# Performance work log

Hardware: AMD Instinct MI355X
Metric: run time of the kernel (lower is better)

## Reference

```python
import jax, jax.numpy as jnp
import numpy as np

# dims matching init_kwargs
L, D, NH = 4, 1024, 16          # num_blocks, embed_dim, num_heads
HD = D // NH                     # head dim
CUR, MEM, BS, IN = 512, 512, 8, 512
FF = 4 * D
GRU_BIAS = 2.0

def sinusoidal_pe(full_seq, dim):
    # SinusoidalPE: freqs = arange(0, dim, 2); inv = 10000**(-freqs/dim); seq descending
    freqs = jnp.arange(0, dim, 2.0)
    inv = 10000.0 ** (-freqs / dim)
    seq = jnp.arange(full_seq - 1, -1, -1.0)
    ang = seq[:, None] * inv[None, :]                       # (full, dim/2)
    return jnp.concatenate([jnp.sin(ang), jnp.cos(ang)], axis=-1)  # (full, dim)

def layer_norm(x, g, b, eps=1e-5):
    m = x.mean(-1, keepdims=True)
    v = ((x - m) ** 2).mean(-1, keepdims=True)
    return (x - m) * jax.lax.rsqrt(v + eps) * g + b

def rel_shift(x):
    # Transformer-XL relative shift. x: (q, k, b, h)
    q, k, b, h = x.shape
    zp = jnp.zeros((q, 1, b, h), x.dtype)
    return jnp.concatenate([zp, x], axis=1).reshape(k + 1, q, b, h)[1:].reshape(q, k, b, h)

def gru_gate(x, y, W):
    # W: (6, D, D) = Wr, Ur, Wz, Uz, Wg, Ug (no bias except learned-ish gru_bias on z)
    Wr, Ur, Wz, Uz, Wg, Ug = W[0], W[1], W[2], W[3], W[4], W[5]
    r = jax.nn.sigmoid(y @ Wr.T + x @ Ur.T)
    z = jax.nn.sigmoid(y @ Wz.T + x @ Uz.T - GRU_BIAS)
    hh = jnp.tanh(y @ Wg.T + (r * x) @ Ug.T)
    return (1.0 - z) * x + z * hh

def rel_attn(q, k, v, pos, U, V, mask, W):
    # q: (cur, bs, D); k, v: (full, bs, D); pos: (full, D); W: (5, D, D) = Wq,Wk,Wv,Wr,Wo
    cur, bs, _ = q.shape
    full = k.shape[0]
    qh = (q @ W[0].T).reshape(cur, bs, NH, HD)
    kh = (k @ W[1].T).reshape(full, bs, NH, HD)
    vh = (v @ W[2].T).reshape(full, bs, NH, HD)
    rh = (pos @ W[3].T).reshape(full, NH, HD)
    AC = jnp.einsum('ibhd,jbhd->ijbh', qh + U, kh)          # content stream with U bias
    BD = rel_shift(jnp.einsum('ibhd,jhd->ijbh', qh + V, rh))  # position stream with V bias
    score = (AC + BD) * (1.0 / np.sqrt(HD))
    score = jnp.where(mask[:, :, None, None], jnp.asarray(-1e30, score.dtype), score)
    attn = jax.nn.softmax(score, axis=1)
    out = jnp.einsum('ijbh,jbhd->ibhd', attn, vh).reshape(cur, bs, D)
    return out @ W[4].T

def gelu(x):
    return jax.nn.gelu(x, approximate=False)  # torch nn.GELU default is exact

def _forward(h, memory, W_emb, b_emb, U, V, ln1, ln2, Wattn, g1, g2, fc_W1, fc_b1, fc_W2, fc_b2):
    h = jnp.transpose(h, (1, 0, 2))            # (cur, bs, in)
    mem = jax.lax.stop_gradient(memory)        # memory holds detached hidden states
    cur = h.shape[0]
    prev = mem.shape[1]
    full = cur + prev
    x = gelu(h @ W_emb.T + b_emb)              # linear embedding + GELU activation
    pos = sinusoidal_pe(full, D)               # (full, D); pos_emb.unsqueeze(1) broadcast over bs
    mask = jnp.triu(jnp.ones((cur, full), bool), 1 + prev)
    out = x
    for i in range(L):
        key = jnp.concatenate([mem[i], out], axis=0)   # (full, bs, D)
        nq = layer_norm(out, ln1[i, 0], ln1[i, 1])
        nk = layer_norm(key, ln1[i, 0], ln1[i, 1])
        Y = rel_attn(nq, nk, nk, pos, U, V, mask, Wattn[i])
        Y = gelu(Y)                                     # dropout is identity (eval / p=0)
        o1 = gru_gate(out, Y, g1[i])
        E = layer_norm(o1, ln2[i, 0], ln2[i, 1])
        E = gelu(gelu(E @ fc_W1[i].T + fc_b1[i]) @ fc_W2[i].T + fc_b2[i])
        out = gru_gate(o1, E, g2[i])
    return jnp.transpose(out, (1, 0, 2))       # (bs, cur, D)

def setup_inputs() -> dict:
    key = jax.random.key(0)
    ks = jax.random.split(key, 12)
    s = 0.02
    eye2 = jnp.stack([jnp.ones(D, jnp.float32), jnp.zeros(D, jnp.float32)])  # (gamma, beta)
    return {
        'h': jax.random.normal(ks[0], (BS, CUR, IN), jnp.float32),
        'memory': jax.random.normal(ks[1], (L, MEM, BS, D), jnp.float32),
        'W_emb': jax.random.normal(ks[2], (D, IN), jnp.float32) * s,
        'b_emb': jnp.zeros((D,), jnp.float32),
        'U': jax.random.normal(ks[3], (NH, HD), jnp.float32) * s,
        'V': jax.random.normal(ks[4], (NH, HD), jnp.float32) * s,
        'ln1': jnp.tile(eye2[None], (L, 1, 1)),
        'ln2': jnp.tile(eye2[None], (L, 1, 1)),
        'Wattn': jax.random.normal(ks[5], (L, 5, D, D), jnp.float32) * s,  # q,k,v,r,o per block
        'g1': jax.random.normal(ks[6], (L, 6, D, D), jnp.float32) * s,
        'g2': jax.random.normal(ks[7], (L, 6, D, D), jnp.float32) * s,
        'fc_W1': jax.random.normal(ks[8], (L, FF, D), jnp.float32) * s,
        'fc_b1': jnp.zeros((L, FF), jnp.float32),
        'fc_W2': jax.random.normal(ks[9], (L, D, FF), jnp.float32) * s,
        'fc_b2': jnp.zeros((L, D), jnp.float32),
    }

def reference(h, memory, W_emb, b_emb, U, V, ln1, ln2, Wattn, g1, g2, fc_W1, fc_b1, fc_W2, fc_b2):
    return _forward(h, memory, W_emb, b_emb, U, V, ln1, ln2, Wattn, g1, g2, fc_W1, fc_b1, fc_W2, fc_b2)
```

## Files before the change

### kernel.cpp

```cpp
#include <hip/hip_runtime.h>
#include <hip/hip_bf16.h>


typedef __attribute__((ext_vector_type(8))) __bf16 bfrag;
typedef __attribute__((ext_vector_type(4))) float f4;
typedef __attribute__((ext_vector_type(4))) unsigned short u16x4;
typedef __attribute__((ext_vector_type(8))) unsigned short u16x8;

__device__ __forceinline__ unsigned short f2bf(float f){
  union { float f; unsigned u; } v; v.f = f;
  unsigned r = v.u + 0x7fffu + ((v.u >> 16) & 1u);
  return (unsigned short)(r >> 16);
}
__device__ __forceinline__ float bf2f(unsigned short u){
  union { unsigned u; float f; } v; v.u = (unsigned)u << 16; return v.f;
}
__device__ __forceinline__ float geluf(float x){
  return 0.5f * x * (1.0f + erff(x * 0.7071067811865476f));
}
__device__ __forceinline__ float sigm(float x){ return 1.0f/(1.0f + __expf(-x)); }

__device__ __forceinline__ void gl_lds(const void* g, void* l){
  __builtin_amdgcn_global_load_lds(
    reinterpret_cast<const __attribute__((address_space(1))) unsigned int*>(
        reinterpret_cast<unsigned long>(g)),
    reinterpret_cast<__attribute__((address_space(3))) unsigned int*>(
        reinterpret_cast<unsigned long>(l)),
    16, 0, 0);
}

struct GP {
  const unsigned short* A;
  const unsigned short* A2;
  const unsigned short* B;
  const unsigned short* B2;
  unsigned short* O1;
  unsigned short* O2;
  unsigned short* O3;
  unsigned short* O4;
  unsigned short* O5;
  float* OF;
  const float* bias1;
  const float* bias2;
  const float* X;
  const float* Z;
  int K, Ksplit, lda, ldb, ldo;
  int sBz;
};

template<int BM, int BN, int EPI>
__global__ __launch_bounds__(256) void gemm_k(GP p){
  __shared__ unsigned short As[2][2][BM*32];
  __shared__ unsigned short Bs[2][2][BN*32];
  const int tid  = threadIdx.x;
  const int lane = tid & 63;
  const int wid  = tid >> 6;
  const int lr   = lane & 15;
  const int lg   = lane >> 4;
  constexpr int FM = BM/32, FN = BN/32;

  int bx = blockIdx.x, by = blockIdx.y;
  {
    const int gx = gridDim.x;
    const int nwg = gx * gridDim.y;
    if ((nwg & 7) == 0){
      const int bid = by*gx + bx;
      const int vid = (bid & 7)*(nwg >> 3) + (bid >> 3);
      bx = vid % gx;
      by = vid / gx;
    }
  }
  const int m0 = by * BM;
  const int n0 = bx * BN;
  const int z  = blockIdx.z;

  const unsigned short* Abase = p.A;
  const unsigned short* Bbase = p.B;
  if constexpr (EPI==13){
    if (z==2){ if (by >= 32) return; Abase = p.A + 4194304; }
    if (z==3){ if (by >= 8)  return; Abase = p.A2; }
    const int zsel = (z==0)?1:((z==1)?2:((z==2)?0:3));
    Bbase = p.B + (long)zsel*1048576;
  }

  const int ksp = p.Ksplit ? p.Ksplit : p.K;
  const unsigned short* AbL = Abase + (long)m0*p.lda;
  const unsigned short* AbH = p.A2 && EPI!=13 ? (p.A2 + (long)m0*p.lda - ksp) : AbL;
  const unsigned short* BbL = Bbase + (long)z*p.sBz + (long)n0*p.ldb;
  const unsigned short* BbH = p.B2 ? (p.B2 + (long)z*p.sBz + (long)n0*p.ldb - ksp) : BbL;

  const int srow = tid >> 2;
  const int skk  = (tid & 3) * 8;

  f4 acc[FM][FN];
  f4 zero4 = {0.0f, 0.0f, 0.0f, 0.0f};
  #pragma unroll
  for (int m=0;m<FM;m++)
    #pragma unroll
    for (int n=0;n<FN;n++) acc[m][n] = zero4;

  auto stage = [&](int buf, int sub, int k0){
    const unsigned short* A_ = (k0 < ksp) ? AbL : AbH;
    #pragma unroll
    for (int q=0;q<BM/64;q++)
      gl_lds(A_ + (long)(q*64 + srow)*p.lda + k0 + skk, (char*)As[buf][sub] + q*4096 + wid*1024);
    const unsigned short* B_ = (k0 < ksp) ? BbL : BbH;
    #pragma unroll
    for (int q=0;q<BN/64;q++)
      gl_lds(B_ + (long)(q*64 + srow)*p.ldb + k0 + skk, (char*)Bs[buf][sub] + q*4096 + wid*1024);
  };

  const int nk2 = p.K >> 6;
  stage(0,0,0); stage(0,1,32);
  __syncthreads();

  int cur = 0;
  for (int t = 0; t < nk2; ++t){
    if (t+1 < nk2){
      stage(cur^1, 0, (t+1)*64);
      stage(cur^1, 1, (t+1)*64 + 32);
    }
    #pragma unroll
    for (int sub=0; sub<2; ++sub){
      bfrag af[FM], bfr[FN];
      #pragma unroll
      for (int m=0;m<FM;m++)
        af[m] = *(const bfrag*)&As[cur][sub][((wid>>1)*(BM/2) + m*16 + lr)*32 + lg*8];
      #pragma unroll
      for (int n=0;n<FN;n++)
        bfr[n] = *(const bfrag*)&Bs[cur][sub][((wid&1)*(BN/2) + n*16 + lr)*32 + lg*8];
      #pragma unroll
      for (int m=0;m<FM;m++)
        #pragma unroll
        for (int n=0;n<FN;n++)
          acc[m][n] = __builtin_amdgcn_mfma_f32_16x16x32_bf16(af[m], bfr[n], acc[m][n], 0, 0, 0);
    }
    __syncthreads();
    cur ^= 1;
  }

  const int wr0 = m0 + (wid>>1)*(BM/2);
  const int wc0 = n0 + (wid&1)*(BN/2);
  #pragma unroll
  for (int m=0;m<FM;m++)
    #pragma unroll
    for (int n=0;n<FN;n++)
      #pragma unroll
      for (int r=0;r<4;r++){
        const int gr = wr0 + m*16 + lg*4 + r;
        const int gc = wc0 + n*16 + lr;
        const float a = acc[m][n][r];
        const long base = (long)gr*p.ldo + gc;
        if constexpr (EPI==6){
          const float t = a + (p.bias1 ? p.bias1[gc] : 0.0f);
          p.O1[base] = f2bf(geluf(t));
        }
        else if constexpr (EPI==7){
          const float t = geluf(a + p.bias1[gc]);
          p.OF[base] = t; p.O1[base] = f2bf(t);
        }
        else if constexpr (EPI==11){
          const long ix = (long)gr*1024 + gc;
          if (z==0) p.O1[ix] = f2bf(sigm(a) * p.X[ix]);
          else      p.OF[ix] = sigm(a - 2.0f);
        }
        else if constexpr (EPI==12){
          const long ix = (long)gr*1024 + gc;
          const float zz = p.Z[ix];
          const float oo = (1.0f - zz)*p.X[ix] + zz*tanhf(a);
          p.OF[ix] = oo; p.O1[ix] = f2bf(oo);
        }
        else if constexpr (EPI==13){
          const long ix = (long)gr*1024 + gc;
          if (z==0){ p.O1[ix] = f2bf(a); }
          else if (z==1){
            const int b_ = gr & 7, js = gr >> 3, h_ = gc >> 6, d_ = gc & 63;
            p.O2[(long)(b_*16 + h_)*65536 + (long)d_*1024 + js] = f2bf(a);
          }
          else if (z==2){ p.O3[ix] = f2bf((a + p.bias1[gc])*0.125f);
                          p.O4[ix] = f2bf((a + p.bias2[gc])*0.125f); }
          else { p.O5[ix] = f2bf(a); }
        }
      }
}

__global__ __launch_bounds__(256,3) void attn_k(const unsigned short* __restrict__ qU,
                                                const unsigned short* __restrict__ qV,
                                                const unsigned short* __restrict__ kh,
                                                const unsigned short* __restrict__ rh,
                                                const unsigned short* __restrict__ vhT,
                                                unsigned short* __restrict__ ctx){
  __shared__ char Sm[20480];
  __shared__ float redm[4][16];
  __shared__ float reds[4][16];
  __shared__ float invd[16];
  const int tid = threadIdx.x;
  const int w   = tid >> 6;
  const int lane= tid & 63;
  const int lr  = lane & 15;
  const int lg  = lane >> 4;
  const int id = blockIdx.x;
  const int b  = id & 7;
  const int i0 = ((id >> 3) & 31) * 16;
  const int h  = id >> 8;
  const int gmax = i0 >> 4;
  const long hoff = (long)h * 64;
  const f4 z4 = {0.f,0.f,0.f,0.f};

  bfrag bqv[2];
  #pragma unroll
  for (int kk=0;kk<2;kk++)
    bqv[kk] = *(const bfrag*)(qV + ((long)(i0 + lr)*8 + b)*1024 + hoff + kk*32 + lg*8);
  bfrag aq[2];
  #pragma unroll
  for (int kk=0;kk<2;kk++)
    aq[kk] = *(const bfrag*)(qU + ((long)(i0 + lr)*8 + b)*1024 + hoff + kk*32 + lg*8);

  const int nv1 = (gmax >= w) ? (((gmax - w) >> 2) + 1) : 0;

  f4 s[16];

#define LDK(DST, n_) { \
    const int cbx = c0 + (w + 4*(n_))*16; \
    DST[0] = *(const bfrag*)(kh + ((long)(cbx + lr)*8 + b)*1024 + hoff + lg*8); \
    DST[1] = *(const bfrag*)(kh + ((long)(cbx + lr)*8 + b)*1024 + hoff + 32 + lg*8); }

#define AC_CMP(n_, CUR) { \
    const int cbx = c0 + (w + 4*(n_))*16; \
    f4 a = z4; \
    __builtin_amdgcn_s_setprio(1); \
    a = __builtin_amdgcn_mfma_f32_16x16x32_bf16(aq[0], CUR[0], a, 0,0,0); \
    a = __builtin_amdgcn_mfma_f32_16x16x32_bf16(aq[1], CUR[1], a, 0,0,0); \
    __builtin_amdgcn_s_setprio(0); \
    _Pragma("unroll") \
    for (int q=0;q<4;q++){ \
      const int di = lg*4 + q; \
      const int jc = cbx + lr; \
      if (jc > i0 + di + 512) a[q] = -1e30f; \
      else { \
        const int rr = jc - di + radd; \
        a[q] += bf2f(*(const unsigned short*)(Sm + rr*38 + di*2)); \
      } \
    } \
    s[half*8 + n_] = a; }

#define AC_STEP(n_, CUR, NXT) \
    if ((n_)+2 < nv) LDK(NXT, (n_)+2); \
    if ((n_) < nv) AC_CMP(n_, CUR) \
    else s[half*8 + n_] = (f4){-1e30f,-1e30f,-1e30f,-1e30f};

  #pragma unroll
  for (int half=0; half<2; ++half){
    const int c0    = half*512;
    const int rbase = half ? (1008 - i0) : (496 - i0);
    const int ntil  = half ? (gmax + 1) : 33;
    const int radd  = half ? -497 : 15;
    for (int mt = w; mt < ntil; mt += 4){
      const int r0 = rbase + mt*16;
      f4 acc = z4;
      #pragma unroll
      for (int kk=0;kk<2;kk++){
        bfrag ar = *(const bfrag*)(rh + (long)(r0 + lr)*1024 + hoff + kk*32 + lg*8);
        acc = __builtin_amdgcn_mfma_f32_16x16x32_bf16(ar, bqv[kk], acc, 0,0,0);
      }
      #pragma unroll
      for (int q=0;q<4;q++){
        const int rr = mt*16 + lg*4 + q;
        *(unsigned short*)(Sm + rr*38 + lr*2) = f2bf(acc[q]);
      }
    }
    __syncthreads();
    const int nv = (half==0) ? 8 : nv1;
    {
      bfrag bkA[2], bkB[2], bkC[2];
      if (0 < nv) LDK(bkA, 0);
      if (1 < nv) LDK(bkB, 1);
      AC_STEP(0, bkA, bkC)
      AC_STEP(1, bkB, bkA)
      AC_STEP(2, bkC, bkB)
      AC_STEP(3, bkA, bkC)
      AC_STEP(4, bkB, bkA)
      AC_STEP(5, bkC, bkB)
      AC_STEP(6, bkA, bkC)
      AC_STEP(7, bkB, bkA)
    }
    __syncthreads();
  }

  const unsigned short* vb_base = vhT + (long)(b*16 + h)*65536;

#define LDV(DST, t_) { \
    const int c0v = ((t_) >> 2) * 512; \
    const int tau = (t_) & 3; \
    const int jA = c0v + (w + 8*tau)*16; \
    const int jB = c0v + (w + 8*tau + 4)*16; \
    const int jcol = (lg < 2) ? (jA + lg*8) : (jB + (lg-2)*8); \
    _Pragma("unroll") \
    for (int nd=0; nd<4; nd++) \
      DST[nd] = *(const bfrag*)(vb_base + (long)(nd*16 + lr)*1024 + jcol); }

#define CHV(t_) ((t_) < 4 || (2*((t_)-4) < nv1))

  bfrag vbA[4], vbB[4];
  LDV(vbA, 0);

  float mx[4], sum[4];
  #pragma unroll
  for (int q=0;q<4;q++){
    float m = s[0][q];
    #pragma unroll
    for (int n=1;n<16;n++) m = fmaxf(m, s[n][q]);
    m = fmaxf(m, __shfl_xor(m, 1));
    m = fmaxf(m, __shfl_xor(m, 2));
    m = fmaxf(m, __shfl_xor(m, 4));
    m = fmaxf(m, __shfl_xor(m, 8));
    if (lr == 0) redm[w][lg*4+q] = m;
  }
  __syncthreads();
  #pragma unroll
  for (int q=0;q<4;q++){
    const int row = lg*4+q;
    mx[q] = fmaxf(fmaxf(redm[0][row], redm[1][row]), fmaxf(redm[2][row], redm[3][row]));
    sum[q] = 0.0f;
  }
  #pragma unroll
  for (int n=0;n<16;n++)
    #pragma unroll
    for (int q=0;q<4;q++){
      const float e = __expf(s[n][q] - mx[q]);
      s[n][q] = e;
      sum[q] += e;
    }
  #pragma unroll
  for (int q=0;q<4;q++){
    float v = sum[q];
    v += __shfl_xor(v, 1);
    v += __shfl_xor(v, 2);
    v += __shfl_xor(v, 4);
    v += __shfl_xor(v, 8);
    if (lr == 0) reds[w][lg*4+q] = v;
  }
  __syncthreads();
  if (tid < 16)
    invd[tid] = 1.0f / (reds[0][tid] + reds[1][tid] + reds[2][tid] + reds[3][tid]);

  f4 oac[4];
  #pragma unroll
  for (int nd=0;nd<4;nd++) oac[nd] = z4;
  char* Pch = Sm + w*1024;

#define PV_STEP(t_, CUR, NXT) \
    if ((t_)+1 < 8 && CHV((t_)+1)) LDV(NXT, (t_)+1); \
    if (CHV(t_)){ \
      const int s0i = (((t_)<4)?0:8) + ((t_)&3)*2; \
      _Pragma("unroll") \
      for (int nn=0;nn<2;nn++){ \
        const f4 e = s[s0i + nn]; \
        _Pragma("unroll") \
        for (int q=0;q<4;q++){ \
          const int row = lg*4 + q; \
          const int col = nn*16 + lr; \
          *(unsigned short*)(Pch + row*64 + ((col*2) ^ (((row>>2)&3)<<4))) = f2bf(e[q]); \
        } \
      } \
      bfrag pa = *(const bfrag*)(Pch + lr*64 + ((lg*16) ^ (((lr>>2)&3)<<4))); \
      __builtin_amdgcn_s_setprio(1); \
      _Pragma("unroll") \
      for (int nd=0;nd<4;nd++) \
        oac[nd] = __builtin_amdgcn_mfma_f32_16x16x32_bf16(pa, CUR[nd], oac[nd], 0,0,0); \
      __builtin_amdgcn_s_setprio(0); \
    }

  PV_STEP(0, vbA, vbB)
  PV_STEP(1, vbB, vbA)
  PV_STEP(2, vbA, vbB)
  PV_STEP(3, vbB, vbA)
  PV_STEP(4, vbA, vbB)
  PV_STEP(5, vbB, vbA)
  PV_STEP(6, vbA, vbB)
  PV_STEP(7, vbB, vbA)

  float* po = (float*)(Sm + 4096 + w*4096);
  #pragma unroll
  for (int nd=0;nd<4;nd++)
    #pragma unroll
    for (int q=0;q<4;q++)
      po[(lg*4+q)*64 + nd*16 + lr] = oac[nd][q];
  __syncthreads();
  {
    const int row = tid >> 4;
    const int d0  = (tid & 15) * 4;
    f4 v = *(const f4*)(Sm + 4096 + (row*64 + d0)*4);
    #pragma unroll
    for (int ww=1;ww<4;ww++){
      const f4 u = *(const f4*)(Sm + 4096 + ww*4096 + (row*64 + d0)*4);
      v.x += u.x; v.y += u.y; v.z += u.z; v.w += u.w;
    }
    const float iv = invd[row];
    u16x4 o;
    o.x = f2bf(v.x*iv); o.y = f2bf(v.y*iv); o.z = f2bf(v.z*iv); o.w = f2bf(v.w*iv);
    *(u16x4*)(ctx + ((long)(i0 + row)*8 + b)*1024 + hoff + d0) = o;
  }
#undef LDK
#undef AC_CMP
#undef AC_STEP
#undef LDV
#undef CHV
#undef PV_STEP
}

__global__ __launch_bounds__(256) void ln_k(const float* __restrict__ srcA,
                                            const float* __restrict__ srcB, int splitRow,
                                            const float* __restrict__ g, const float* __restrict__ b,
                                            unsigned short* __restrict__ dst){
  const int row = blockIdx.x;
  const float* src = (srcB != nullptr && row >= splitRow)
                       ? (srcB + (long)(row - splitRow)*1024)
                       : (srcA + (long)row*1024);
  const int t = threadIdx.x;
  float4 v = ((const float4*)src)[t];
  float s1 = v.x+v.y+v.z+v.w;
  float s2 = v.x*v.x+v.y*v.y+v.z*v.z+v.w*v.w;
  #pragma unroll
  for (int o=32;o;o>>=1){ s1 += __shfl_xor(s1,o); s2 += __shfl_xor(s2,o); }
  __shared__ float r1[4], r2[4];
  const int w = t>>6;
  if ((t&63)==0){ r1[w]=s1; r2[w]=s2; }
  __syncthreads();
  s1 = r1[0]+r1[1]+r1[2]+r1[3];
  s2 = r2[0]+r2[1]+r2[2]+r2[3];
  const float mean = s1*(1.0f/1024.0f);
  const float var  = s2*(1.0f/1024.0f) - mean*mean;
  const float rs   = rsqrtf(var + 1e-5f);
  float4 gg = ((const float4*)g)[t];
  float4 bb = ((const float4*)b)[t];
  u16x4 o;
  o.x = f2bf((v.x-mean)*rs*gg.x + bb.x);
  o.y = f2bf((v.y-mean)*rs*gg.y + bb.y);
  o.z = f2bf((v.z-mean)*rs*gg.z + bb.z);
  o.w = f2bf((v.w-mean)*rs*gg.w + bb.w);
  *(u16x4*)(dst + (long)row*1024 + t*4) = o;
}

__global__ __launch_bounds__(256) void conv_k(const float* __restrict__ s,
                                              unsigned short* __restrict__ d, long n){
  long i = ((long)blockIdx.x*256 + threadIdx.x)*4;
  if (i >= n) return;
  float4 v = *(const float4*)(s + i);
  u16x4 o; o.x=f2bf(v.x); o.y=f2bf(v.y); o.z=f2bf(v.z); o.w=f2bf(v.w);
  *(u16x4*)(d + i) = o;
}

__global__ __launch_bounds__(256) void conv5_k(const float* __restrict__ wat,
                                               const float* __restrict__ g1,
                                               const float* __restrict__ g2,
                                               const float* __restrict__ f1,
                                               const float* __restrict__ f2,
                                               unsigned short* __restrict__ dst){
  const long i = ((long)blockIdx.x*256 + threadIdx.x)*4;
  const float* s; long off;
  if      (i <  5242880){ s = wat; off = 0; }
  else if (i < 11534336){ s = g1;  off = 5242880; }
  else if (i < 17825792){ s = g2;  off = 11534336; }
  else if (i < 22020096){ s = f1;  off = 17825792; }
  else                  { s = f2;  off = 22020096; }
  float4 v = *(const float4*)(s + (i - off));
  u16x4 o; o.x=f2bf(v.x); o.y=f2bf(v.y); o.z=f2bf(v.z); o.w=f2bf(v.w);
  *(u16x4*)(dst + i) = o;
}

__global__ __launch_bounds__(128) void ht_k(const float* __restrict__ h,
                                            unsigned short* __restrict__ d){
  const int row = blockIdx.x;
  const int i = row>>3, b = row&7;
  const float* src = h + ((long)b*512 + i)*512;
  const int t = threadIdx.x;
  float4 v = ((const float4*)src)[t];
  u16x4 o; o.x=f2bf(v.x); o.y=f2bf(v.y); o.z=f2bf(v.z); o.w=f2bf(v.w);
  *(u16x4*)(d + (long)row*512 + t*4) = o;
}

__global__ __launch_bounds__(256) void pos_k(unsigned short* __restrict__ d){
  const int r = blockIdx.x, t = threadIdx.x;
  const float seq = (float)(1023 - r);
  u16x4 o;
  #pragma unroll
  for (int q=0;q<4;q++){
    const int c = t*4 + q;
    const int f = (c < 512) ? c : (c - 512);
    const float inv = expf((float)f * -0.017988946039016f);
    const float ang = seq * inv;
    const float val = (c < 512) ? sinf(ang) : cosf(ang);
    o[q] = f2bf(val);
  }
  *(u16x4*)(d + (long)r*1024 + t*4) = o;
}

__global__ __launch_bounds__(256) void outT_k(const float* __restrict__ o,
                                              float* __restrict__ d){
  const int row = blockIdx.x;
  const int b = row>>9, i = row&511;
  const float4 v = ((const float4*)(o + ((long)i*8 + b)*1024))[threadIdx.x];
  ((float4*)(d + (long)row*1024))[threadIdx.x] = v;
}

extern "C" void kernel_launch(void* const* d_in, const int* in_sizes, int n_in,
                              void* d_out, int out_size, void* d_ws, size_t ws_size,
                              hipStream_t stream){
  (void)in_sizes; (void)n_in; (void)out_size; (void)ws_size;
  const float* h     = (const float*)d_in[0];
  const float* memin = (const float*)d_in[1];
  const float* Wemb  = (const float*)d_in[2];
  const float* bemb  = (const float*)d_in[3];
  const float* Ub    = (const float*)d_in[4];
  const float* Vb    = (const float*)d_in[5];
  const float* ln1   = (const float*)d_in[6];
  const float* ln2   = (const float*)d_in[7];
  const float* Wattn = (const float*)d_in[8];
  const float* g1w   = (const float*)d_in[9];
  const float* g2w   = (const float*)d_in[10];
  const float* fw1   = (const float*)d_in[11];
  const float* fb1   = (const float*)d_in[12];
  const float* fw2   = (const float*)d_in[13];
  const float* fb2   = (const float*)d_in[14];

  char* Wp = (char*)d_ws;
  size_t off = 0;
  auto take = [&](size_t bytes)->size_t{ size_t r = off; off += (bytes + 255) & ~(size_t)255; return r; };
  float*          outf = (float*)         (Wp + take(16777216));
  unsigned short* xbf  = (unsigned short*)(Wp + take( 8388608));
  float*          o1f  = (float*)         (Wp + take(16777216));
  unsigned short* o1b  = (unsigned short*)(Wp + take( 8388608));
  float*          zbf  = (float*)         (Wp + take(16777216));
  unsigned short* rxb  = (unsigned short*)(Wp + take( 8388608));
  unsigned short* yb   = (unsigned short*)(Wp + take( 8388608));
  unsigned short* Eb   = (unsigned short*)(Wp + take( 8388608));
  unsigned short* wb0  = (unsigned short*)(Wp + take(52428800));
  unsigned short* hTb  = (unsigned short*)(Wp + take( 4194304));
  unsigned short* webb = (unsigned short*)(Wp + take( 1048576));
  unsigned short* posb = (unsigned short*)(Wp + take( 2097152));
  unsigned short* nkb  = (unsigned short*)(Wp + take(16777216));
  unsigned short* qUb  = (unsigned short*)(Wp + take( 8388608));
  unsigned short* qVb  = (unsigned short*)(Wp + take( 8388608));
  unsigned short* khb  = (unsigned short*)(Wp + take(16777216));
  unsigned short* vhTb = (unsigned short*)(Wp + take(16777216));
  unsigned short* F1b  = khb;
  unsigned short* rhb  = (unsigned short*)(Wp + take( 2097152));
  unsigned short* ctxb = (unsigned short*)(Wp + take( 8388608));

  const int M1 = 1048576;

  conv_k<<<512, 256, 0, stream>>>(Wemb, webb, 524288);
  ht_k<<<4096, 128, 0, stream>>>(h, hTb);
  pos_k<<<1024, 256, 0, stream>>>(posb);

  {
    GP p{}; p.A=hTb; p.B=webb; p.OF=outf; p.O1=xbf; p.bias1=bemb;
    p.K=512; p.lda=512; p.ldb=512; p.ldo=1024;
    gemm_k<128,64,7><<<dim3(16,32,1),256,0,stream>>>(p);
  }

  auto gru_fn = [&](const unsigned short* xb, const float* xf, const unsigned short* yb_,
                    const unsigned short* w6, float* of, unsigned short* ob){
    { GP p{}; p.A=yb_; p.A2=xb; p.B=w6; p.B2=w6+M1; p.sBz=2*M1;
      p.O1=rxb; p.OF=zbf; p.X=xf;
      p.K=2048; p.Ksplit=1024; p.lda=1024; p.ldb=1024; p.ldo=1024;
      gemm_k<128,64,11><<<dim3(16,32,2),256,0,stream>>>(p); }
    { GP p{}; p.A=yb_; p.A2=rxb; p.B=w6+4*M1; p.B2=w6+5*M1;
      p.X=xf; p.Z=zbf; p.OF=of; p.O1=ob;
      p.K=2048; p.Ksplit=1024; p.lda=1024; p.ldb=1024; p.ldo=1024;
      gemm_k<128,64,12><<<dim3(16,32,1),256,0,stream>>>(p); }
  };

  for (int l = 0; l < 4; ++l){
    conv5_k<<<25600,256,0,stream>>>(Wattn + (long)l*5242880,
                                    g1w   + (long)l*6291456,
                                    g2w   + (long)l*6291456,
                                    fw1   + (long)l*4194304,
                                    fw2   + (long)l*4194304, wb0);

    ln_k<<<8192,256,0,stream>>>(memin + (long)l*4194304, outf, 4096,
                                ln1 + l*2048, ln1 + l*2048 + 1024, nkb);

    {
      GP p{}; p.A=nkb; p.A2=posb; p.B=wb0;
      p.O1=khb; p.O2=vhTb; p.O3=qUb; p.O4=qVb; p.O5=rhb;
      p.bias1=Ub; p.bias2=Vb;
      p.K=1024; p.lda=1024; p.ldb=1024; p.ldo=1024;
      gemm_k<128,64,13><<<dim3(16,64,4),256,0,stream>>>(p); }

    attn_k<<<4096,256,0,stream>>>(qUb, qVb, khb, rhb, vhTb, ctxb);

    {
      GP p{}; p.A=ctxb; p.B=wb0+4*M1; p.O1=yb;
      p.K=1024; p.lda=1024; p.ldb=1024; p.ldo=1024;
      gemm_k<128,64,6><<<dim3(16,32,1),256,0,stream>>>(p); }

    gru_fn(xbf, outf, yb, wb0 + 5*M1, o1f, o1b);

    ln_k<<<4096,256,0,stream>>>(o1f, nullptr, 1<<30,
                                ln2 + l*2048, ln2 + l*2048 + 1024, Eb);

    { GP p{}; p.A=Eb;  p.B=wb0+17*M1; p.O1=F1b; p.bias1=fb1 + l*4096;
      p.K=1024; p.lda=1024; p.ldb=1024; p.ldo=4096;
      gemm_k<128,64,6><<<dim3(64,32,1),256,0,stream>>>(p); }
    { GP p{}; p.A=F1b; p.B=wb0+21*M1; p.O1=yb; p.bias1=fb2 + l*1024;
      p.K=4096; p.lda=4096; p.ldb=4096; p.ldo=1024;
      gemm_k<128,64,6><<<dim3(16,32,1),256,0,stream>>>(p); }

    gru_fn(o1b, o1f, yb, wb0 + 11*M1, outf, xbf);
  }

  outT_k<<<4096,256,0,stream>>>(outf, (float*)d_out);
}
```

Measured before the change: 2.693 ms.

## Keep residual stream in bf16 and fuse final transpose into GRU epilogue

The fp32 copies of the residual stream (outf, o1f) and the z gate are replaced by bf16 buffers. GRU epilogues and layer norms now read bf16. The last GRU gate writes the transposed fp32 output straight to the result buffer, so the separate transpose kernel goes away. This cuts memory traffic in the epilogues and the LN loads, but the residual path now carries bf16 rounding across all layers, which can hurt accuracy.

```diff
diff --git a/kernel.cpp b/kernel.cpp
--- a/kernel.cpp
+++ b/kernel.cpp
@@ -42,8 +42,8 @@
   float* OF;
   const float* bias1;
   const float* bias2;
-  const float* X;
-  const float* Z;
+  const unsigned short* XB;
+  const unsigned short* ZB;
   int K, Ksplit, lda, ldb, ldo;
   int sBz;
 };
@@ -155,20 +155,23 @@
           const float t = a + (p.bias1 ? p.bias1[gc] : 0.0f);
           p.O1[base] = f2bf(geluf(t));
         }
-        else if constexpr (EPI==7){
-          const float t = geluf(a + p.bias1[gc]);
-          p.OF[base] = t; p.O1[base] = f2bf(t);
-        }
         else if constexpr (EPI==11){
           const long ix = (long)gr*1024 + gc;
-          if (z==0) p.O1[ix] = f2bf(sigm(a) * p.X[ix]);
-          else      p.OF[ix] = sigm(a - 2.0f);
+          if (z==0) p.O1[ix] = f2bf(sigm(a) * bf2f(p.XB[ix]));
+          else      p.O2[ix] = f2bf(sigm(a - 2.0f));
         }
         else if constexpr (EPI==12){
           const long ix = (long)gr*1024 + gc;
-          const float zz = p.Z[ix];
-          const float oo = (1.0f - zz)*p.X[ix] + zz*tanhf(a);
-          p.OF[ix] = oo; p.O1[ix] = f2bf(oo);
+          const float zz = bf2f(p.ZB[ix]);
+          const float oo = (1.0f - zz)*bf2f(p.XB[ix]) + zz*tanhf(a);
+          p.O1[ix] = f2bf(oo);
+        }
+        else if constexpr (EPI==14){
+          const long ix = (long)gr*1024 + gc;
+          const float zz = bf2f(p.ZB[ix]);
+          const float oo = (1.0f - zz)*bf2f(p.XB[ix]) + zz*tanhf(a);
+          const int i_ = gr >> 3, b_ = gr & 7;
+          p.OF[(long)b_*524288 + (long)i_*1024 + gc] = oo;
         }
         else if constexpr (EPI==13){
           const long ix = (long)gr*1024 + gc;
@@ -410,15 +413,18 @@
 }
 
 __global__ __launch_bounds__(256) void ln_k(const float* __restrict__ srcA,
-                                            const float* __restrict__ srcB, int splitRow,
+                                            const unsigned short* __restrict__ srcB, int splitRow,
                                             const float* __restrict__ g, const float* __restrict__ b,
                                             unsigned short* __restrict__ dst){
   const int row = blockIdx.x;
-  const float* src = (srcB != nullptr && row >= splitRow)
-                       ? (srcB + (long)(row - splitRow)*1024)
-                       : (srcA + (long)row*1024);
   const int t = threadIdx.x;
-  float4 v = ((const float4*)src)[t];
+  float4 v;
+  if (row < splitRow){
+    v = ((const float4*)(srcA + (long)row*1024))[t];
+  } else {
+    u16x4 uv = *(const u16x4*)(srcB + (long)(row - splitRow)*1024 + t*4);
+    v.x = bf2f(uv.x); v.y = bf2f(uv.y); v.z = bf2f(uv.z); v.w = bf2f(uv.w);
+  }
   float s1 = v.x+v.y+v.z+v.w;
   float s2 = v.x*v.x+v.y*v.y+v.z*v.z+v.w*v.w;
   #pragma unroll
@@ -494,14 +500,6 @@
     o[q] = f2bf(val);
   }
   *(u16x4*)(d + (long)r*1024 + t*4) = o;
-}
-
-__global__ __launch_bounds__(256) void outT_k(const float* __restrict__ o,
-                                              float* __restrict__ d){
-  const int row = blockIdx.x;
-  const int b = row>>9, i = row&511;
-  const float4 v = ((const float4*)(o + ((long)i*8 + b)*1024))[threadIdx.x];
-  ((float4*)(d + (long)row*1024))[threadIdx.x] = v;
 }
 
 extern "C" void kernel_launch(void* const* d_in, const int* in_sizes, int n_in,
@@ -527,11 +525,9 @@
   char* Wp = (char*)d_ws;
   size_t off = 0;
   auto take = [&](size_t bytes)->size_t{ size_t r = off; off += (bytes + 255) & ~(size_t)255; return r; };
-  float*          outf = (float*)         (Wp + take(16777216));
   unsigned short* xbf  = (unsigned short*)(Wp + take( 8388608));
-  float*          o1f  = (float*)         (Wp + take(16777216));
   unsigned short* o1b  = (unsigned short*)(Wp + take( 8388608));
-  float*          zbf  = (float*)         (Wp + take(16777216));
+  unsigned short* zbb  = (unsigned short*)(Wp + take( 8388608));
   unsigned short* rxb  = (unsigned short*)(Wp + take( 8388608));
   unsigned short* yb   = (unsigned short*)(Wp + take( 8388608));
   unsigned short* Eb   = (unsigned short*)(Wp + take( 8388608));
@@ -555,21 +551,22 @@
   pos_k<<<1024, 256, 0, stream>>>(posb);
 
   {
-    GP p{}; p.A=hTb; p.B=webb; p.OF=outf; p.O1=xbf; p.bias1=bemb;
+    GP p{}; p.A=hTb; p.B=webb; p.O1=xbf; p.bias1=bemb;
     p.K=512; p.lda=512; p.ldb=512; p.ldo=1024;
-    gemm_k<128,64,7><<<dim3(16,32,1),256,0,stream>>>(p);
-  }
-
-  auto gru_fn = [&](const unsigned short* xb, const float* xf, const unsigned short* yb_,
-                    const unsigned short* w6, float* of, unsigned short* ob){
+    gemm_k<128,64,6><<<dim3(16,32,1),256,0,stream>>>(p);
+  }
+
+  auto gru_fn = [&](const unsigned short* xb, const unsigned short* yb_,
+                    const unsigned short* w6, unsigned short* ob, float* of, bool last){
     { GP p{}; p.A=yb_; p.A2=xb; p.B=w6; p.B2=w6+M1; p.sBz=2*M1;
-      p.O1=rxb; p.OF=zbf; p.X=xf;
+      p.O1=rxb; p.O2=zbb; p.XB=xb;
       p.K=2048; p.Ksplit=1024; p.lda=1024; p.ldb=1024; p.ldo=1024;
       gemm_k<128,64,11><<<dim3(16,32,2),256,0,stream>>>(p); }
-    { GP p{}; p.A=yb_; p.A2=rxb; p.B=w6+4*M1; p.B2=w6+5*M1;
-      p.X=xf; p.Z=zbf; p.OF=of; p.O1=ob;
-      p.K=2048; p.Ksplit=1024; p.lda=1024; p.ldb=1024; p.ldo=1024;
-      gemm_k<128,64,12><<<dim3(16,32,1),256,0,stream>>>(p); }
+    GP p{}; p.A=yb_; p.A2=rxb; p.B=w6+4*M1; p.B2=w6+5*M1;
+    p.XB=xb; p.ZB=zbb; p.O1=ob; p.OF=of;
+    p.K=2048; p.Ksplit=1024; p.lda=1024; p.ldb=1024; p.ldo=1024;
+    if (last) gemm_k<128,64,14><<<dim3(16,32,1),256,0,stream>>>(p);
+    else      gemm_k<128,64,12><<<dim3(16,32,1),256,0,stream>>>(p);
   };
 
   for (int l = 0; l < 4; ++l){
@@ -579,7 +576,7 @@
                                     fw1   + (long)l*4194304,
                                     fw2   + (long)l*4194304, wb0);
 
-    ln_k<<<8192,256,0,stream>>>(memin + (long)l*4194304, outf, 4096,
+    ln_k<<<8192,256,0,stream>>>(memin + (long)l*4194304, xbf, 4096,
                                 ln1 + l*2048, ln1 + l*2048 + 1024, nkb);
 
     {
@@ -596,9 +593,9 @@
       p.K=1024; p.lda=1024; p.ldb=1024; p.ldo=1024;
       gemm_k<128,64,6><<<dim3(16,32,1),256,0,stream>>>(p); }
 
-    gru_fn(xbf, outf, yb, wb0 + 5*M1, o1f, o1b);
-
-    ln_k<<<4096,256,0,stream>>>(o1f, nullptr, 1<<30,
+    gru_fn(xbf, yb, wb0 + 5*M1, o1b, nullptr, false);
+
+    ln_k<<<4096,256,0,stream>>>(nullptr, o1b, 0,
                                 ln2 + l*2048, ln2 + l*2048 + 1024, Eb);
 
     { GP p{}; p.A=Eb;  p.B=wb0+17*M1; p.O1=F1b; p.bias1=fb1 + l*4096;
@@ -608,8 +605,6 @@
       p.K=4096; p.lda=4096; p.ldb=4096; p.ldo=1024;
       gemm_k<128,64,6><<<dim3(16,32,1),256,0,stream>>>(p); }
 
-    gru_fn(o1b, o1f, yb, wb0 + 11*M1, outf, xbf);
-  }
-
-  outT_k<<<4096,256,0,stream>>>(outf, (float*)d_out);
-}
+    gru_fn(o1b, yb, wb0 + 11*M1, xbf, (float*)d_out, l==3);
+  }
+}
```

Result: no change. 2.682 ms, median of 2 (-0.4%).
